# Performance work log

Measured on AMD Instinct MI355X. Metric: run time of the kernel, lower is better.

The kernel has to match this reference:

```python
import jax, jax.numpy as jnp
import numpy as np

N = 8192       # node_num
F_IN = 256     # src_feature
F_OUT = 128    # out_feature
NEG_SLOPE = 0.2  # standard GAT leakyrelu slope
MASK_VAL = -1e12


def setup_inputs() -> dict:
    key = jax.random.key(0)
    k1, k2, k3, k4, k5, k6 = jax.random.split(key, 6)
    x = jax.random.normal(k1, (N, F_IN), dtype=jnp.float32)
    adj = jax.random.randint(k2, (N, N), 0, 2, dtype=jnp.int32)  # 0/1 adjacency mask
    # xavier-uniform-like scales
    W = jax.random.normal(k3, (F_IN, F_OUT), dtype=jnp.float32) * np.float32(1.0 / np.sqrt(F_IN))
    a1 = jax.random.normal(k4, (F_OUT,), dtype=jnp.float32) * np.float32(0.1)  # att[:F_OUT]
    a2 = jax.random.normal(k5, (F_OUT,), dtype=jnp.float32) * np.float32(0.1)  # att[F_OUT:]
    bias = jax.random.normal(k6, (F_OUT,), dtype=jnp.float32) * np.float32(0.1)
    return {"x": x, "adj": adj, "W": W, "a1": a1, "a2": a2, "bias": bias}


def reference(x, adj, W, a1, a2, bias):
    # h = x @ W1  (src_h == dst_h for int src_dst_feature)
    h = x @ W  # [N, F_OUT]
    # e[i,j] = leakyrelu(att^T [h_i || h_j]) decomposed as (h@a1)_i + (h@a2)_j
    s_src = h @ a1  # [N]
    s_dst = h @ a2  # [N]
    e = jax.nn.leaky_relu(s_src[:, None] + s_dst[None, :], NEG_SLOPE)  # [N, N]
    masked = jnp.where(adj > 0, e, jnp.float32(MASK_VAL))
    attention = jax.nn.softmax(masked, axis=1)  # [N, N]
    # dropout in eval mode = identity; aggregate neighbor features
    out = attention @ h + bias  # [N, F_OUT]
    return out
```

## Files before the change

### kernel.cpp

```cpp
#include <hip/hip_runtime.h>
#include <cstdint>
#include <cstddef>

#define NN 8192
#define FIN 256
#define FOUT 128
#define SLOPE 0.2f
#define SHIFT 8.0f

typedef float f32x4 __attribute__((ext_vector_type(4)));
typedef __bf16 bf16x8 __attribute__((ext_vector_type(8)));
typedef int i32x4 __attribute__((ext_vector_type(4)));
typedef unsigned int u32x4 __attribute__((ext_vector_type(4)));

__device__ __forceinline__ unsigned short f2bf(float f) {
  return __builtin_bit_cast(unsigned short, (__bf16)f);
}

__device__ __forceinline__ void async_cp16(void* lds, const void* g) {
  __builtin_amdgcn_global_load_lds(
      (const __attribute__((address_space(1))) void*)g,
      (__attribute__((address_space(3))) void*)lds, 16, 0, 0);
}

__global__ __launch_bounds__(256, 4) void k_hw(const float* __restrict__ x,
                                               const float* __restrict__ W,
                                               const float* __restrict__ a1,
                                               const float* __restrict__ a2,
                                               unsigned short* __restrict__ ht,
                                               float* __restrict__ Etab,
                                               unsigned short* __restrict__ FbfF,
                                               unsigned short* __restrict__ FbfF2,
                                               float* __restrict__ outacc,
                                               float* __restrict__ dws) {
  __shared__ float xs[8][256];
  __shared__ unsigned short tile[128][8];
  const int tid = threadIdx.x;
  const int rowbase = blockIdx.x * 8;

  {
    f32x4 z = {0.f, 0.f, 0.f, 0.f};
    *(f32x4*)(outacc + (size_t)blockIdx.x * 1024 + tid * 4) = z;
    if (tid < 2) *(f32x4*)(dws + blockIdx.x * 8 + tid * 4) = z;
  }

  #pragma unroll
  for (int it = 0; it < 2; ++it) {
    int fi = it * 1024 + tid * 4;
    int r = fi >> 8, k = fi & 255;
    *(f32x4*)&xs[r][k] = *(const f32x4*)(x + (size_t)(rowbase + r) * FIN + k);
  }
  __syncthreads();

  const int r = tid >> 5;
  const int cg = tid & 31;
  f32x4 acc = {0.f, 0.f, 0.f, 0.f};

  #pragma unroll 8
  for (int k = 0; k < FIN; ++k) {
    f32x4 wv = *(const f32x4*)(W + k * FOUT + cg * 4);
    float xv = xs[r][k];
    acc[0] += xv * wv[0];
    acc[1] += xv * wv[1];
    acc[2] += xv * wv[2];
    acc[3] += xv * wv[3];
  }

  #pragma unroll
  for (int c = 0; c < 4; ++c) tile[cg * 4 + c][r] = f2bf(acc[c]);

  f32x4 av1 = *(const f32x4*)(a1 + cg * 4);
  f32x4 av2 = *(const f32x4*)(a2 + cg * 4);
  float s1 = acc[0] * av1[0] + acc[1] * av1[1] + acc[2] * av1[2] + acc[3] * av1[3];
  float s2 = acc[0] * av2[0] + acc[1] * av2[1] + acc[2] * av2[2] + acc[3] * av2[3];
  #pragma unroll
  for (int off = 16; off > 0; off >>= 1) {
    s1 += __shfl_xor(s1, off, 64);
    s2 += __shfl_xor(s2, off, 64);
  }
  if (cg == 0) {
    const int row = rowbase + r;
    float c0 = s1 + SHIFT;
    float c = fmaxf(c0, SLOPE * c0);
    Etab[(size_t)row * 2]     = __expf(s1 - c);
    Etab[(size_t)row * 2 + 1] = __expf(SLOPE * s1 - c);
    FbfF[row]  = f2bf(__expf(s2));
    FbfF2[row] = f2bf(__expf(SLOPE * s2));
  }
  __syncthreads();

  if (tid < 128) {
    u32x4 v = *(const u32x4*)&tile[tid][0];
    *(u32x4*)(ht + (size_t)tid * NN + rowbase) = v;
  }
}

__global__ __launch_bounds__(256, 4) void k_gat(const int* __restrict__ adj,
                                                const unsigned short* __restrict__ ht,
                                                const float* __restrict__ Etab,
                                                const unsigned short* __restrict__ FbfF,
                                                const unsigned short* __restrict__ FbfF2,
                                                float* __restrict__ outacc,
                                                float* __restrict__ dws) {
  __shared__ int sA[2][16 * 64];
  __shared__ unsigned short sH[2][128 * 64];

  const int tid = threadIdx.x;
  const int wave = tid >> 6;
  const int lane = tid & 63;
  const int quad = lane >> 4;
  const int m = lane & 15;
  const int rowbase = (int)(blockIdx.x >> 1) * 16;
  const int colbase = (int)(blockIdx.x & 1) * (NN / 2);
  const int row = rowbase + m;

  bf16x8 pm, pinv, pones;
  #pragma unroll
  for (int jj = 0; jj < 8; ++jj) {
    pm[jj] = (__bf16)(float)m;
    pinv[jj] = (__bf16)0.03125f;
    pones[jj] = (__bf16)1.0f;
  }
  f32x4 z = {0.f, 0.f, 0.f, 0.f};
  f32x4 rp = __builtin_amdgcn_mfma_f32_16x16x32_bf16(pm, pinv, z, 0, 0, 0);
  f32x4 cp = __builtin_amdgcn_mfma_f32_16x16x32_bf16(pinv, pm, z, 0, 0, 0);
  int rowmap[4], colmap[4];
  #pragma unroll
  for (int r = 0; r < 4; ++r) {
    rowmap[r] = ((int)(rp[r] + 0.5f)) & 15;
    colmap[r] = ((int)(cp[r] + 0.5f)) & 15;
  }

  const float E  = Etab[(size_t)row * 2];
  const float E2 = Etab[(size_t)row * 2 + 1];
  const int t0 = wave * 2, t1 = wave * 2 + 1;

  f32x4 acc0 = z, acc1 = z, den = z;

  const unsigned short* srcH[4];
  #pragma unroll
  for (int il = 0; il < 4; ++il) {
    const int i = wave * 4 + il;
    const int f = i * 8 + (lane >> 3);
    const int g = (lane & 7) ^ (lane >> 3);
    srcH[il] = ht + (size_t)f * NN + colbase + g * 8;
  }
  const int* srcA[2] = {nullptr, nullptr};
  int slotA[2] = {0, 0};
  if (wave >= 2) {
    #pragma unroll
    for (int q2 = 0; q2 < 2; ++q2) {
      const int il = (wave - 2) * 2 + q2;
      const int r = il * 4 + (lane >> 4);
      const int g = (lane & 15) ^ r;
      slotA[q2] = il;
      srcA[q2] = adj + (size_t)(rowbase + r) * NN + colbase + g * 4;
    }
  }

  auto stage = [&](int b) {
    #pragma unroll
    for (int il = 0; il < 4; ++il) {
      async_cp16(&sH[b][(wave * 4 + il) * 512], srcH[il]);
      srcH[il] += 64;
    }
    if (wave >= 2) {
      #pragma unroll
      for (int q2 = 0; q2 < 2; ++q2) {
        async_cp16(&sA[b][slotA[q2] * 256], srcA[q2]);
        srcA[q2] += 64;
      }
    }
  };

  const unsigned short* fbase = FbfF  + colbase + quad * 8;
  const unsigned short* gbase = FbfF2 + colbase + quad * 8;
  struct Fregs { u32x4 F0, F1, G0, G1; };
  auto load_f = [&](Fregs& d, int c) {
    const unsigned short* p = fbase + c * 64;
    const unsigned short* q = gbase + c * 64;
    d.F0 = *(const u32x4*)(p);
    d.F1 = *(const u32x4*)(p + 32);
    d.G0 = *(const u32x4*)(q);
    d.G1 = *(const u32x4*)(q + 32);
  };

  auto compute = [&](int cs, const Fregs& fr) {
    #pragma unroll
    for (int k32 = 0; k32 < 2; ++k32) {
      const int g0 = k32 * 8 + quad * 2;
      i32x4 A0 = *(const i32x4*)&sA[cs][m * 64 + ((g0) ^ m) * 4];
      i32x4 A1 = *(const i32x4*)&sA[cs][m * 64 + ((g0 + 1) ^ m) * 4];
      const u32x4 Fq = k32 ? fr.F1 : fr.F0;
      const u32x4 Gq = k32 ? fr.G1 : fr.G0;

      bf16x8 af;
      #pragma unroll
      for (int p = 0; p < 4; ++p) {
        const unsigned fp = Fq[p], gp = Gq[p];
        const float Flo = __builtin_bit_cast(float, fp << 16);
        const float Fhi = __builtin_bit_cast(float, fp & 0xffff0000u);
        const float Glo = __builtin_bit_cast(float, gp << 16);
        const float Ghi = __builtin_bit_cast(float, gp & 0xffff0000u);
        const float wlo = fmaxf(E * Flo, E2 * Glo);
        const float whi = fmaxf(E * Fhi, E2 * Ghi);
        const int avlo = (p < 2) ? A0[p * 2] : A1[p * 2 - 4];
        const int avhi = (p < 2) ? A0[p * 2 + 1] : A1[p * 2 - 3];
        af[p * 2]     = avlo ? (__bf16)wlo : (__bf16)0.0f;
        af[p * 2 + 1] = avhi ? (__bf16)whi : (__bf16)0.0f;
      }

      const int s0 = (k32 * 4 + quad) ^ (m & 7);
      bf16x8 b0 = __builtin_bit_cast(bf16x8,
          *(const u32x4*)&sH[cs][(t0 * 16 + m) * 64 + s0 * 8]);
      bf16x8 b1 = __builtin_bit_cast(bf16x8,
          *(const u32x4*)&sH[cs][(t1 * 16 + m) * 64 + s0 * 8]);

      acc0 = __builtin_amdgcn_mfma_f32_16x16x32_bf16(af, b0, acc0, 0, 0, 0);
      acc1 = __builtin_amdgcn_mfma_f32_16x16x32_bf16(af, b1, acc1, 0, 0, 0);
      den  = __builtin_amdgcn_mfma_f32_16x16x32_bf16(af, pones, den, 0, 0, 0);
    }
  };

  Fregs fA, fB;
  load_f(fA, 0);
  stage(0);

  #pragma unroll 1
  for (int c = 0; c < 64; c += 2) {
    __syncthreads();
    stage(1);
    load_f(fB, c + 1);
    compute(0, fA);
    __syncthreads();
    if (c + 2 < 64) {
      stage(0);
      load_f(fA, c + 2);
    }
    compute(1, fB);
  }

  #pragma unroll
  for (int r = 0; r < 4; ++r) {
    const int orow = rowbase + rowmap[r];
    const int c0 = t0 * 16 + colmap[r];
    const int c1 = t1 * 16 + colmap[r];
    atomicAdd(&outacc[(size_t)orow * FOUT + c0], acc0[r]);
    atomicAdd(&outacc[(size_t)orow * FOUT + c1], acc1[r]);
  }
  if (wave == 0 && m == 0) {
    #pragma unroll
    for (int r = 0; r < 4; ++r) {
      atomicAdd(&dws[rowbase + rowmap[r]], den[r]);
    }
  }
}

__global__ __launch_bounds__(256) void k_fin(const float* __restrict__ dws,
                                             const float* __restrict__ bias,
                                             float* __restrict__ out) {
  const int idx = (blockIdx.x * 256 + threadIdx.x) * 4;
  const int rowi = idx >> 7;
  const int f = idx & 127;
  const float inv = 1.0f / dws[rowi];
  f32x4 v = *(f32x4*)(out + idx);
  f32x4 b = *(const f32x4*)(bias + f);
  v[0] = v[0] * inv + b[0];
  v[1] = v[1] * inv + b[1];
  v[2] = v[2] * inv + b[2];
  v[3] = v[3] * inv + b[3];
  *(f32x4*)(out + idx) = v;
}

extern "C" void kernel_launch(void* const* d_in, const int* in_sizes, int n_in,
                              void* d_out, int out_size, void* d_ws, size_t ws_size,
                              hipStream_t stream) {
  const float* x    = (const float*)d_in[0];
  const int*   adj  = (const int*)d_in[1];
  const float* W    = (const float*)d_in[2];
  const float* a1   = (const float*)d_in[3];
  const float* a2   = (const float*)d_in[4];
  const float* bias = (const float*)d_in[5];
  float* out = (float*)d_out;

  char* ws = (char*)d_ws;
  unsigned short* ht = (unsigned short*)ws;
  float* Etab = (float*)(ws + (size_t)2 * 1024 * 1024);
  unsigned short* FbfF =
      (unsigned short*)(ws + (size_t)2 * 1024 * 1024 + 64 * 1024);
  unsigned short* FbfF2 = FbfF + NN;
  float* dws = (float*)(ws + (size_t)2 * 1024 * 1024 + 96 * 1024);

  k_hw<<<NN / 8, 256, 0, stream>>>(x, W, a1, a2, ht, Etab, FbfF, FbfF2, out, dws);
  k_gat<<<(NN / 16) * 2, 256, 0, stream>>>(adj, ht, Etab, FbfF, FbfF2, out, dws);
  k_fin<<<(NN * FOUT / 4) / 256, 256, 0, stream>>>(dws, bias, out);
}
```

Measured before the change: 464.8 us.

## Deepen adjacency prefetch to four stages and stage F tables through LDS

Restructures the main loop of the GAT aggregation kernel so adjacency tiles are prefetched three chunks ahead in a 4-deep LDS ring. The H tiles stay double-buffered, and the bf16 exp tables F/F2 are now copied asynchronously into LDS instead of loaded into registers. Synchronization uses raw s_barrier plus per-wave s_waitcnt vmcnt counts tuned to each wave's outstanding loads, in place of __syncthreads. The goal is to hide global-memory latency on the adjacency stream, which is the dominant traffic. The cost is more LDS, occupancy lowered from 4 to 3 blocks, and fragile hand-counted wait counts.

```diff
diff --git a/kernel.cpp b/kernel.cpp
--- a/kernel.cpp
+++ b/kernel.cpp
@@ -95,15 +95,16 @@
   }
 }
 
-__global__ __launch_bounds__(256, 4) void k_gat(const int* __restrict__ adj,
+__global__ __launch_bounds__(256, 3) void k_gat(const int* __restrict__ adj,
                                                 const unsigned short* __restrict__ ht,
                                                 const float* __restrict__ Etab,
                                                 const unsigned short* __restrict__ FbfF,
                                                 const unsigned short* __restrict__ FbfF2,
                                                 float* __restrict__ outacc,
                                                 float* __restrict__ dws) {
-  __shared__ int sA[2][16 * 64];
+  __shared__ int sA[4][16 * 64];
   __shared__ unsigned short sH[2][128 * 64];
+  __shared__ unsigned short sF[2][128];
 
   const int tid = threadIdx.x;
   const int wave = tid >> 6;
@@ -137,15 +138,15 @@
 
   f32x4 acc0 = z, acc1 = z, den = z;
 
-  const unsigned short* srcH[4];
+  const unsigned short* htb[4];
   #pragma unroll
   for (int il = 0; il < 4; ++il) {
     const int i = wave * 4 + il;
     const int f = i * 8 + (lane >> 3);
     const int g = (lane & 7) ^ (lane >> 3);
-    srcH[il] = ht + (size_t)f * NN + colbase + g * 8;
-  }
-  const int* srcA[2] = {nullptr, nullptr};
+    htb[il] = ht + (size_t)f * NN + colbase + g * 8;
+  }
+  const int* adb[2] = {nullptr, nullptr};
   int slotA[2] = {0, 0};
   if (wave >= 2) {
     #pragma unroll
@@ -154,45 +155,38 @@
       const int r = il * 4 + (lane >> 4);
       const int g = (lane & 15) ^ r;
       slotA[q2] = il;
-      srcA[q2] = adj + (size_t)(rowbase + r) * NN + colbase + g * 4;
-    }
-  }
-
-  auto stage = [&](int b) {
-    #pragma unroll
-    for (int il = 0; il < 4; ++il) {
-      async_cp16(&sH[b][(wave * 4 + il) * 512], srcH[il]);
-      srcH[il] += 64;
-    }
+      adb[q2] = adj + (size_t)(rowbase + r) * NN + colbase + g * 4;
+    }
+  }
+  const unsigned short* fbp =
+      (lane < 8) ? (FbfF + colbase + lane * 8) : (FbfF2 + colbase + (lane - 8) * 8);
+
+  auto stageH = [&](int buf, int cidx) {
+    #pragma unroll
+    for (int il = 0; il < 4; ++il)
+      async_cp16(&sH[buf][(wave * 4 + il) * 512], htb[il] + cidx * 64);
+  };
+  auto stageF = [&](int buf, int cidx) {
+    if (wave == 1 && lane < 16) async_cp16(&sF[buf][0], fbp + cidx * 64);
+  };
+  auto stageA = [&](int buf, int cidx) {
     if (wave >= 2) {
       #pragma unroll
-      for (int q2 = 0; q2 < 2; ++q2) {
-        async_cp16(&sA[b][slotA[q2] * 256], srcA[q2]);
-        srcA[q2] += 64;
-      }
-    }
-  };
-
-  const unsigned short* fbase = FbfF  + colbase + quad * 8;
-  const unsigned short* gbase = FbfF2 + colbase + quad * 8;
-  struct Fregs { u32x4 F0, F1, G0, G1; };
-  auto load_f = [&](Fregs& d, int c) {
-    const unsigned short* p = fbase + c * 64;
-    const unsigned short* q = gbase + c * 64;
-    d.F0 = *(const u32x4*)(p);
-    d.F1 = *(const u32x4*)(p + 32);
-    d.G0 = *(const u32x4*)(q);
-    d.G1 = *(const u32x4*)(q + 32);
-  };
-
-  auto compute = [&](int cs, const Fregs& fr) {
+      for (int q2 = 0; q2 < 2; ++q2)
+        async_cp16(&sA[buf][slotA[q2] * 256], adb[q2] + cidx * 64);
+    }
+  };
+
+  auto compute = [&](int c) {
+    const int bh = c & 1, ba = c & 3;
     #pragma unroll
     for (int k32 = 0; k32 < 2; ++k32) {
       const int g0 = k32 * 8 + quad * 2;
-      i32x4 A0 = *(const i32x4*)&sA[cs][m * 64 + ((g0) ^ m) * 4];
-      i32x4 A1 = *(const i32x4*)&sA[cs][m * 64 + ((g0 + 1) ^ m) * 4];
-      const u32x4 Fq = k32 ? fr.F1 : fr.F0;
-      const u32x4 Gq = k32 ? fr.G1 : fr.G0;
+      i32x4 A0 = *(const i32x4*)&sA[ba][m * 64 + ((g0) ^ m) * 4];
+      i32x4 A1 = *(const i32x4*)&sA[ba][m * 64 + ((g0 + 1) ^ m) * 4];
+      const int jl = k32 * 32 + quad * 8;
+      u32x4 Fq = *(const u32x4*)&sF[bh][jl];
+      u32x4 Gq = *(const u32x4*)&sF[bh][64 + jl];
 
       bf16x8 af;
       #pragma unroll
@@ -212,9 +206,9 @@
 
       const int s0 = (k32 * 4 + quad) ^ (m & 7);
       bf16x8 b0 = __builtin_bit_cast(bf16x8,
-          *(const u32x4*)&sH[cs][(t0 * 16 + m) * 64 + s0 * 8]);
+          *(const u32x4*)&sH[bh][(t0 * 16 + m) * 64 + s0 * 8]);
       bf16x8 b1 = __builtin_bit_cast(bf16x8,
-          *(const u32x4*)&sH[cs][(t1 * 16 + m) * 64 + s0 * 8]);
+          *(const u32x4*)&sH[bh][(t1 * 16 + m) * 64 + s0 * 8]);
 
       acc0 = __builtin_amdgcn_mfma_f32_16x16x32_bf16(af, b0, acc0, 0, 0, 0);
       acc1 = __builtin_amdgcn_mfma_f32_16x16x32_bf16(af, b1, acc1, 0, 0, 0);
@@ -222,23 +216,29 @@
     }
   };
 
-  Fregs fA, fB;
-  load_f(fA, 0);
-  stage(0);
+  stageH(0, 0);
+  stageF(0, 0);
+  stageA(0, 0);
+  stageA(1, 1);
+  stageA(2, 2);
 
   #pragma unroll 1
-  for (int c = 0; c < 64; c += 2) {
-    __syncthreads();
-    stage(1);
-    load_f(fB, c + 1);
-    compute(0, fA);
-    __syncthreads();
-    if (c + 2 < 64) {
-      stage(0);
-      load_f(fA, c + 2);
-    }
-    compute(1, fB);
-  }
+  for (int c = 0; c < 64; ++c) {
+    __builtin_amdgcn_s_barrier();
+    const int cn = (c + 1 < 64) ? c + 1 : 63;
+    const int ca = (c + 3 < 64) ? c + 3 : 63;
+    stageH((c + 1) & 1, cn);
+    stageF((c + 1) & 1, cn);
+    stageA((c + 3) & 3, ca);
+    if (wave >= 2)      asm volatile("s_waitcnt vmcnt(10)" ::: "memory");
+    else if (wave == 1) asm volatile("s_waitcnt vmcnt(5)"  ::: "memory");
+    else                asm volatile("s_waitcnt vmcnt(4)"  ::: "memory");
+    __builtin_amdgcn_s_barrier();
+    __builtin_amdgcn_sched_barrier(0);
+    compute(c);
+  }
+
+  asm volatile("s_waitcnt vmcnt(0)" ::: "memory");
 
   #pragma unroll
   for (int r = 0; r < 4; ++r) {
```

New measurement: 480.6 us. 3.4% more time.
